# Performance work log

Hardware: AMD Instinct MI355X
Metric: run time of the kernel (lower is better)

## Reference

```python
import jax, jax.numpy as jnp
import numpy as np

NUM_GRAPHS = 256
N_NODES = 100000
N_EDGES = 1200000
NODE_DIM = 64
NUM_LAYERS = 3
R_HID = 128
R_OUT = 32


def setup_inputs() -> dict:
    key = jax.random.key(0)
    ks = jax.random.split(key, 10)
    x = jax.random.normal(ks[0], (N_NODES, NODE_DIM), dtype=jnp.float32)
    src = jax.random.randint(ks[1], (N_EDGES,), 0, N_NODES)
    dst = jax.random.randint(ks[2], (N_EDGES,), 0, N_NODES)
    graph_ids = jnp.sort(jax.random.randint(ks[3], (N_NODES,), 0, NUM_GRAPHS))
    s = 1.0 / np.sqrt(NODE_DIM)
    gin_W = jax.random.normal(ks[4], (NUM_LAYERS, NODE_DIM, NODE_DIM), dtype=jnp.float32) * s
    gin_b = jnp.zeros((NUM_LAYERS, NODE_DIM), dtype=jnp.float32)
    eps = jnp.zeros((NUM_LAYERS,), dtype=jnp.float32)  # learnable GIN epsilon
    in_dim = NODE_DIM * NUM_LAYERS
    r_W1 = jax.random.normal(ks[5], (in_dim, R_HID), dtype=jnp.float32) / np.sqrt(in_dim)
    r_b1 = jnp.zeros((R_HID,), dtype=jnp.float32)
    r_W2 = jax.random.normal(ks[6], (R_HID, R_OUT), dtype=jnp.float32) / np.sqrt(R_HID)
    r_b2 = jnp.zeros((R_OUT,), dtype=jnp.float32)
    return {"x": x, "gin_W": gin_W, "gin_b": gin_b, "eps": eps,
            "r_W1": r_W1, "r_b1": r_b1, "r_W2": r_W2, "r_b2": r_b2,
            "src": src, "dst": dst, "graph_ids": graph_ids}


def reference(x, gin_W, gin_b, eps, r_W1, r_b1, r_W2, r_b2, src, dst, graph_ids):
    n = x.shape[0]
    h = x
    hs = []
    for l in range(NUM_LAYERS):  # fixed small layer loop
        # neighbor sum aggregation: scatter-add messages h[src] into dst
        agg = jax.ops.segment_sum(h[src], dst, num_segments=n)  # [N, D]
        h = jax.nn.relu(((1.0 + eps[l]) * h + agg) @ gin_W[l] + gin_b[l])
        hs.append(h)
    H = jnp.stack(hs, axis=1)  # [N, L, D]
    # dgl.sum_nodes per layer output == ragged segment-sum over graph ids
    g = jax.ops.segment_sum(H, graph_ids, num_segments=NUM_GRAPHS)  # [B, L, D]
    g = g.reshape(NUM_GRAPHS, -1)  # [B, L*D]
    # readout MLP (2 layers)
    out = jax.nn.relu(g @ r_W1 + r_b1) @ r_W2 + r_b2
    return out
```

## Files before the change

### kernel.cpp

```cpp
#include <hip/hip_runtime.h>


#define SPLIT 16
#define NBLK 512
#define BS 512

typedef unsigned short ushort_t;
typedef __bf16 v8bf __attribute__((ext_vector_type(8)));
typedef float v4f __attribute__((ext_vector_type(4)));

__device__ __forceinline__ float h2f_lo(unsigned int v) {
    return (float)__builtin_bit_cast(_Float16, (unsigned short)(v & 0xffffu));
}
__device__ __forceinline__ float h2f_hi(unsigned int v) {
    return (float)__builtin_bit_cast(_Float16, (unsigned short)(v >> 16));
}
__device__ __forceinline__ unsigned int f2h(float f) {
    return (unsigned int)__builtin_bit_cast(unsigned short, (_Float16)f);
}

__global__ void cast_kernel(const float* __restrict__ x, ushort_t* __restrict__ xh, int n4) {
    int i = blockIdx.x * blockDim.x + threadIdx.x;
    if (i < n4) {
        float4 v = ((const float4*)x)[i];
        uint2 p;
        p.x = f2h(v.x) | (f2h(v.y) << 16);
        p.y = f2h(v.z) | (f2h(v.w) << 16);
        ((uint2*)xh)[i] = p;
    }
}

__global__ void prep_w_kernel(const float* __restrict__ W,
                              ushort_t* __restrict__ whi, ushort_t* __restrict__ wlo,
                              int total) {
    int i = blockIdx.x * blockDim.x + threadIdx.x;
    if (i >= total) return;
    int l = i >> 12, r = i & 4095;
    int n = r >> 6, k = r & 63;
    float w = W[l * 4096 + k * 64 + n];
    __bf16 h = (__bf16)w;
    float rem = w - (float)h;
    __bf16 lo = (__bf16)rem;
    whi[i] = __builtin_bit_cast(ushort_t, h);
    wlo[i] = __builtin_bit_cast(ushort_t, lo);
}

__global__ __launch_bounds__(256) void bucket_count_kernel(
        const int* __restrict__ dst, int* __restrict__ cnt2d,
        int E, int nbkt, int ebpb) {
    __shared__ int lcnt[256];
    int t = threadIdx.x;
    lcnt[t] = 0;
    __syncthreads();
    int base = blockIdx.x * ebpb;
    int end = min(base + ebpb, E);
    for (int i = base + t; i < end; i += 256)
        atomicAdd(&lcnt[dst[i] >> 9], 1);
    __syncthreads();
    if (t < nbkt) cnt2d[(size_t)blockIdx.x * nbkt + t] = lcnt[t];
}

__global__ __launch_bounds__(256) void colscan_kernel(
        const int* __restrict__ cnt2d, int* __restrict__ blkoff,
        int* __restrict__ btot, int nbkt) {
    __shared__ int sh[256];
    int b = blockIdx.x, t = threadIdx.x;
    int i0 = 2 * t, i1 = 2 * t + 1;
    int v0 = cnt2d[(size_t)i0 * nbkt + b];
    int v1 = cnt2d[(size_t)i1 * nbkt + b];
    int pair = v0 + v1;
    sh[t] = pair;
    __syncthreads();
    for (int off = 1; off < 256; off <<= 1) {
        int u = (t >= off) ? sh[t - off] : 0;
        __syncthreads();
        sh[t] += u;
        __syncthreads();
    }
    int ex = sh[t] - pair;
    blkoff[(size_t)b * NBLK + i0] = ex;
    blkoff[(size_t)b * NBLK + i1] = ex + v0;
    if (t == 255) btot[b] = sh[255];
}

__global__ __launch_bounds__(256) void bucket_base_kernel(
        const int* __restrict__ btot, int* __restrict__ bbase,
        int* __restrict__ offsets, int nbkt, int N, int E) {
    __shared__ int sh[256];
    int t = threadIdx.x;
    int v = (t < nbkt) ? btot[t] : 0;
    sh[t] = v;
    __syncthreads();
    for (int off = 1; off < 256; off <<= 1) {
        int u = (t >= off) ? sh[t - off] : 0;
        __syncthreads();
        sh[t] += u;
        __syncthreads();
    }
    if (t < nbkt) bbase[t] = sh[t] - v;
    if (t == 0) { bbase[nbkt] = E; offsets[N] = E; }
}

__global__ __launch_bounds__(256) void bucket_scatter_kernel(
        const int* __restrict__ src, const int* __restrict__ dst,
        const int* __restrict__ bbase, const int* __restrict__ blkoff,
        unsigned int* __restrict__ bkt, int E, int nbkt, int ebpb) {
    __shared__ int lbase[256];
    __shared__ int lrank[256];
    int t = threadIdx.x;
    if (t < nbkt) lbase[t] = bbase[t] + blkoff[(size_t)t * NBLK + blockIdx.x];
    lrank[t] = 0;
    __syncthreads();
    int base = blockIdx.x * ebpb;
    int end = min(base + ebpb, E);
    for (int i = base + t; i < end; i += 256) {
        int d = dst[i];
        int b = d >> 9;
        int r = atomicAdd(&lrank[b], 1);
        bkt[lbase[b] + r] = ((unsigned int)src[i] << 9) | (unsigned int)(d & (BS - 1));
    }
}

__global__ __launch_bounds__(256) void csr_build_kernel(
        const unsigned int* __restrict__ bkt, const int* __restrict__ bbase,
        int* __restrict__ offsets, int* __restrict__ csr, int N, int nbkt) {
    __shared__ int cnt[BS];
    __shared__ int rank[BS];
    __shared__ int sh[256];
    int b = blockIdx.x, t = threadIdx.x;
    cnt[t] = 0; cnt[t + 256] = 0;
    rank[t] = 0; rank[t + 256] = 0;
    __syncthreads();
    int base = bbase[b], end = bbase[b + 1];
    for (int i = base + t; i < end; i += 256)
        atomicAdd(&cnt[bkt[i] & (BS - 1)], 1);
    __syncthreads();
    int i0 = 2 * t, i1 = 2 * t + 1;
    int v0 = cnt[i0], v1 = cnt[i1];
    int pair = v0 + v1;
    sh[t] = pair;
    __syncthreads();
    for (int off = 1; off < 256; off <<= 1) {
        int u = (t >= off) ? sh[t - off] : 0;
        __syncthreads();
        sh[t] += u;
        __syncthreads();
    }
    int ex = sh[t] - pair;
    __syncthreads();
    cnt[i0] = ex;
    cnt[i1] = ex + v0;
    __syncthreads();
    int d0 = (b << 9) + i0;
    if (d0 <= N) offsets[d0] = base + cnt[i0];
    int d1 = (b << 9) + i1;
    if (d1 <= N) offsets[d1] = base + cnt[i1];
    for (int i = base + t; i < end; i += 256) {
        unsigned int v = bkt[i];
        int dl = v & (BS - 1);
        int r = atomicAdd(&rank[dl], 1);
        csr[base + cnt[dl] + r] = (int)(v >> 9);
    }
}

__global__ __launch_bounds__(256) void layer_kernel(
        const ushort_t* __restrict__ hin, ushort_t* __restrict__ hout,
        const int* __restrict__ offsets, const int* __restrict__ csr,
        const ushort_t* __restrict__ wt_hi, const ushort_t* __restrict__ wt_lo,
        const float* __restrict__ gin_b, const float* __restrict__ eps_arr,
        int layer, int N) {
    __shared__ float rows[4 * 16 * 64];
    int t = threadIdx.x;
    int wv = t >> 6, lane = t & 63;
    int tile = blockIdx.x * 4 + wv;
    if (tile * 16 >= N) return;
    float* myrows = rows + wv * 16 * 64;
    float eps1 = 1.0f + eps_arr[layer];

    int nq = lane >> 4;
    int sl = lane & 15;

    #pragma unroll
    for (int p = 0; p < 4; ++p) {
        int node = tile * 16 + p * 4 + nq;
        float ax = 0.f, ay = 0.f, az = 0.f, aw = 0.f;
        if (node < N) {
            int e0 = offsets[node], e1 = offsets[node + 1];
            #pragma unroll 4
            for (int e = e0; e < e1; ++e) {
                int s = csr[e];
                uint2 v = ((const uint2*)(hin + (size_t)s * 64))[sl];
                ax += h2f_lo(v.x); ay += h2f_hi(v.x);
                az += h2f_lo(v.y); aw += h2f_hi(v.y);
            }
            uint2 self = ((const uint2*)(hin + (size_t)node * 64))[sl];
            ax = fmaf(eps1, h2f_lo(self.x), ax);
            ay = fmaf(eps1, h2f_hi(self.x), ay);
            az = fmaf(eps1, h2f_lo(self.y), az);
            aw = fmaf(eps1, h2f_hi(self.y), aw);
        }
        float4 r4; r4.x = ax; r4.y = ay; r4.z = az; r4.w = aw;
        *(float4*)&myrows[(p * 4 + nq) * 64 + sl * 4] = r4;
    }

    int c = lane & 15;
    int q = lane >> 4;
    int node16 = tile * 16 + c;

    const ushort_t* Whi = wt_hi + layer * 4096;
    const ushort_t* Wlo = wt_lo + layer * 4096;
    const float*    bl  = gin_b + layer * 64;

    v8bf bhi[2], blo2[2];
    #pragma unroll
    for (int kt = 0; kt < 2; ++kt) {
        float4 f0 = *(float4*)&myrows[c * 64 + kt * 32 + q * 8];
        float4 f1 = *(float4*)&myrows[c * 64 + kt * 32 + q * 8 + 4];
        float xs[8] = {f0.x, f0.y, f0.z, f0.w, f1.x, f1.y, f1.z, f1.w};
        #pragma unroll
        for (int j = 0; j < 8; ++j) {
            __bf16 h = (__bf16)xs[j];
            bhi[kt][j] = h;
            blo2[kt][j] = (__bf16)(xs[j] - (float)h);
        }
    }

    #pragma unroll
    for (int mt = 0; mt < 4; ++mt) {
        v4f acc = {0.f, 0.f, 0.f, 0.f};
        #pragma unroll
        for (int kt = 0; kt < 2; ++kt) {
            int dim = mt * 16 + c;
            size_t off = (size_t)dim * 64 + kt * 32 + q * 8;
            v8bf ah = __builtin_bit_cast(v8bf, *(const uint4*)(Whi + off));
            v8bf al = __builtin_bit_cast(v8bf, *(const uint4*)(Wlo + off));
            acc = __builtin_amdgcn_mfma_f32_16x16x32_bf16(ah, bhi[kt],  acc, 0, 0, 0);
            acc = __builtin_amdgcn_mfma_f32_16x16x32_bf16(ah, blo2[kt], acc, 0, 0, 0);
            acc = __builtin_amdgcn_mfma_f32_16x16x32_bf16(al, bhi[kt],  acc, 0, 0, 0);
        }
        float4 bv = ((const float4*)(bl + mt * 16))[q];
        float o0 = fmaxf(acc[0] + bv.x, 0.f);
        float o1 = fmaxf(acc[1] + bv.y, 0.f);
        float o2 = fmaxf(acc[2] + bv.z, 0.f);
        float o3 = fmaxf(acc[3] + bv.w, 0.f);
        uint2 pk;
        pk.x = f2h(o0) | (f2h(o1) << 16);
        pk.y = f2h(o2) | (f2h(o3) << 16);
        if (node16 < N)
            *(uint2*)(hout + (size_t)node16 * 64 + mt * 16 + q * 4) = pk;
    }
}

__global__ __launch_bounds__(192) void readout_part_kernel(
        const ushort_t* __restrict__ H, const int* __restrict__ gids,
        float* __restrict__ gpart, int N) {
    int graph = blockIdx.x / SPLIT;
    int sp    = blockIdx.x % SPLIT;
    int lo = 0, hi = N;
    while (lo < hi) { int mid = (lo + hi) >> 1; if (gids[mid] < graph) lo = mid + 1; else hi = mid; }
    int start = lo;
    int lo2 = start, hi2 = N;
    while (lo2 < hi2) { int mid = (lo2 + hi2) >> 1; if (gids[mid] < graph + 1) lo2 = mid + 1; else hi2 = mid; }
    int end = lo2;
    int t = threadIdx.x;
    int l = t >> 6, d = t & 63;
    float acc = 0.0f;
    int cnt = end - start;
    if (cnt > 0) {
        int per = (cnt + SPLIT - 1) / SPLIT;
        int cs = start + sp * per;
        int ce = min(cs + per, end);
        const ushort_t* Hl = H + (size_t)l * N * 64;
        for (int n = cs; n < ce; ++n)
            acc += (float)__builtin_bit_cast(_Float16, Hl[(size_t)n * 64 + d]);
    }
    gpart[(size_t)(graph * SPLIT + sp) * 192 + t] = acc;
}

__global__ __launch_bounds__(192) void mlp_kernel(
        const float* __restrict__ gpart,
        const float* __restrict__ W1, const float* __restrict__ b1,
        const float* __restrict__ W2, const float* __restrict__ b2,
        float* __restrict__ out) {
    __shared__ float gr[192];
    __shared__ float hid[128];
    int graph = blockIdx.x;
    int t = threadIdx.x;
    float a = 0.f;
    #pragma unroll
    for (int sp = 0; sp < SPLIT; ++sp)
        a += gpart[(size_t)(graph * SPLIT + sp) * 192 + t];
    gr[t] = a;
    __syncthreads();
    if (t < 128) {
        float s = b1[t];
        for (int k = 0; k < 192; ++k) s = fmaf(gr[k], W1[k * 128 + t], s);
        hid[t] = fmaxf(s, 0.0f);
    }
    __syncthreads();
    if (t < 32) {
        float s = b2[t];
        for (int k = 0; k < 128; ++k) s = fmaf(hid[k], W2[k * 32 + t], s);
        out[graph * 32 + t] = s;
    }
}

extern "C" void kernel_launch(void* const* d_in, const int* in_sizes, int n_in,
                              void* d_out, int out_size, void* d_ws, size_t ws_size,
                              hipStream_t stream) {
    const float* x     = (const float*)d_in[0];
    const float* gin_W = (const float*)d_in[1];
    const float* gin_b = (const float*)d_in[2];
    const float* eps   = (const float*)d_in[3];
    const float* r_W1  = (const float*)d_in[4];
    const float* r_b1  = (const float*)d_in[5];
    const float* r_W2  = (const float*)d_in[6];
    const float* r_b2  = (const float*)d_in[7];
    const int*   src   = (const int*)d_in[8];
    const int*   dst   = (const int*)d_in[9];
    const int*   gids  = (const int*)d_in[10];

    int N = in_sizes[0] / 64;
    int E = in_sizes[8];
    int B = out_size / 32;

    int nbkt = (N + BS - 1) / BS;
    int ebpb = (E + NBLK - 1) / NBLK;

    int* ws       = (int*)d_ws;
    float* gpart  = (float*)ws;
    int* cnt2d    = ws + (size_t)B * SPLIT * 192;
    int* blkoff   = cnt2d + (size_t)NBLK * nbkt;
    int* btot     = blkoff + (size_t)nbkt * NBLK;
    int* bbase    = btot + nbkt;
    int* offsets  = bbase + (nbkt + 1);
    unsigned int* bkt = (unsigned int*)(offsets + (N + 1));
    int* csr      = (int*)(bkt + E);
    size_t w      = (size_t)(csr + E - ws);
    w = (w + 15) & ~(size_t)15;
    ushort_t* xh  = (ushort_t*)(ws + w);
    ushort_t* H   = xh + (size_t)N * 64;
    ushort_t* whi = H + 3 * (size_t)N * 64;
    ushort_t* wlo = whi + 3 * 4096;

    cast_kernel<<<(N * 64 / 4 + 255) / 256, 256, 0, stream>>>(x, xh, N * 64 / 4);
    prep_w_kernel<<<(3 * 4096 + 255) / 256, 256, 0, stream>>>(gin_W, whi, wlo, 3 * 4096);
    bucket_count_kernel<<<NBLK, 256, 0, stream>>>(dst, cnt2d, E, nbkt, ebpb);
    colscan_kernel<<<nbkt, 256, 0, stream>>>(cnt2d, blkoff, btot, nbkt);
    bucket_base_kernel<<<1, 256, 0, stream>>>(btot, bbase, offsets, nbkt, N, E);
    bucket_scatter_kernel<<<NBLK, 256, 0, stream>>>(src, dst, bbase, blkoff, bkt, E, nbkt, ebpb);
    csr_build_kernel<<<nbkt, 256, 0, stream>>>(bkt, bbase, offsets, csr, N, nbkt);

    int lbk = (N + 63) / 64;
    ushort_t* H0 = H;
    ushort_t* H1 = H + (size_t)N * 64;
    ushort_t* H2 = H + 2 * (size_t)N * 64;

    layer_kernel<<<lbk, 256, 0, stream>>>(xh, H0, offsets, csr, whi, wlo, gin_b, eps, 0, N);
    layer_kernel<<<lbk, 256, 0, stream>>>(H0, H1, offsets, csr, whi, wlo, gin_b, eps, 1, N);
    layer_kernel<<<lbk, 256, 0, stream>>>(H1, H2, offsets, csr, whi, wlo, gin_b, eps, 2, N);

    readout_part_kernel<<<B * SPLIT, 192, 0, stream>>>(H, gids, gpart, N);
    mlp_kernel<<<B, 192, 0, stream>>>(gpart, r_W1, r_b1, r_W2, r_b2, (float*)d_out);
}
```

Baseline: 326.1 us.

## Fuse prep kernels and restructure GIN layer to one tile per block

Merges the cast, weight-prep and bucket-count kernels into a single launch by dispatching on block index, which saves two launches. The layer kernel now gives each block one 16-node tile. Each wave gathers 4 nodes in a single pass instead of looping over 16 serially, then computes one 16-wide output slice of the matmul after a block barrier. Neighbour indices are preloaded cooperatively into registers and broadcast with shuffles. This is meant to raise memory-level parallelism and shorten per-wave latency chains, at the cost of a block barrier and four times as many blocks.

```diff
diff --git a/kernel.cpp b/kernel.cpp
--- a/kernel.cpp
+++ b/kernel.cpp
@@ -19,45 +19,45 @@
     return (unsigned int)__builtin_bit_cast(unsigned short, (_Float16)f);
 }
 
-__global__ void cast_kernel(const float* __restrict__ x, ushort_t* __restrict__ xh, int n4) {
-    int i = blockIdx.x * blockDim.x + threadIdx.x;
-    if (i < n4) {
-        float4 v = ((const float4*)x)[i];
-        uint2 p;
-        p.x = f2h(v.x) | (f2h(v.y) << 16);
-        p.y = f2h(v.z) | (f2h(v.w) << 16);
-        ((uint2*)xh)[i] = p;
-    }
-}
-
-__global__ void prep_w_kernel(const float* __restrict__ W,
-                              ushort_t* __restrict__ whi, ushort_t* __restrict__ wlo,
-                              int total) {
-    int i = blockIdx.x * blockDim.x + threadIdx.x;
-    if (i >= total) return;
-    int l = i >> 12, r = i & 4095;
-    int n = r >> 6, k = r & 63;
-    float w = W[l * 4096 + k * 64 + n];
-    __bf16 h = (__bf16)w;
-    float rem = w - (float)h;
-    __bf16 lo = (__bf16)rem;
-    whi[i] = __builtin_bit_cast(ushort_t, h);
-    wlo[i] = __builtin_bit_cast(ushort_t, lo);
-}
-
-__global__ __launch_bounds__(256) void bucket_count_kernel(
+__global__ __launch_bounds__(256) void pre_kernel(
         const int* __restrict__ dst, int* __restrict__ cnt2d,
-        int E, int nbkt, int ebpb) {
+        int E, int nbkt, int ebpb,
+        const float* __restrict__ x, ushort_t* __restrict__ xh, int n4, int castBlocks,
+        const float* __restrict__ W, ushort_t* __restrict__ whi,
+        ushort_t* __restrict__ wlo, int wtotal) {
     __shared__ int lcnt[256];
     int t = threadIdx.x;
-    lcnt[t] = 0;
-    __syncthreads();
-    int base = blockIdx.x * ebpb;
-    int end = min(base + ebpb, E);
-    for (int i = base + t; i < end; i += 256)
-        atomicAdd(&lcnt[dst[i] >> 9], 1);
-    __syncthreads();
-    if (t < nbkt) cnt2d[(size_t)blockIdx.x * nbkt + t] = lcnt[t];
+    int blk = blockIdx.x;
+    if (blk < NBLK) {
+        lcnt[t] = 0;
+        __syncthreads();
+        int base = blk * ebpb;
+        int end = min(base + ebpb, E);
+        for (int i = base + t; i < end; i += 256)
+            atomicAdd(&lcnt[dst[i] >> 9], 1);
+        __syncthreads();
+        if (t < nbkt) cnt2d[(size_t)blk * nbkt + t] = lcnt[t];
+    } else if (blk < NBLK + castBlocks) {
+        int i = (blk - NBLK) * 256 + t;
+        if (i < n4) {
+            float4 v = ((const float4*)x)[i];
+            uint2 p;
+            p.x = f2h(v.x) | (f2h(v.y) << 16);
+            p.y = f2h(v.z) | (f2h(v.w) << 16);
+            ((uint2*)xh)[i] = p;
+        }
+    } else {
+        int i = (blk - NBLK - castBlocks) * 256 + t;
+        if (i < wtotal) {
+            int l = i >> 12, r = i & 4095;
+            int n = r >> 6, k = r & 63;
+            float w = W[l * 4096 + k * 64 + n];
+            __bf16 h = (__bf16)w;
+            float rem = w - (float)h;
+            whi[i] = __builtin_bit_cast(ushort_t, h);
+            wlo[i] = __builtin_bit_cast(ushort_t, (__bf16)rem);
+        }
+    }
 }
 
 __global__ __launch_bounds__(256) void colscan_kernel(
@@ -169,43 +169,59 @@
         const ushort_t* __restrict__ wt_hi, const ushort_t* __restrict__ wt_lo,
         const float* __restrict__ gin_b, const float* __restrict__ eps_arr,
         int layer, int N) {
-    __shared__ float rows[4 * 16 * 64];
+    __shared__ float rows[16 * 64];
     int t = threadIdx.x;
     int wv = t >> 6, lane = t & 63;
-    int tile = blockIdx.x * 4 + wv;
-    if (tile * 16 >= N) return;
-    float* myrows = rows + wv * 16 * 64;
+    int tile = blockIdx.x;
     float eps1 = 1.0f + eps_arr[layer];
 
     int nq = lane >> 4;
     int sl = lane & 15;
-
-    #pragma unroll
-    for (int p = 0; p < 4; ++p) {
-        int node = tile * 16 + p * 4 + nq;
-        float ax = 0.f, ay = 0.f, az = 0.f, aw = 0.f;
-        if (node < N) {
-            int e0 = offsets[node], e1 = offsets[node + 1];
-            #pragma unroll 4
-            for (int e = e0; e < e1; ++e) {
-                int s = csr[e];
-                uint2 v = ((const uint2*)(hin + (size_t)s * 64))[sl];
-                ax += h2f_lo(v.x); ay += h2f_hi(v.x);
-                az += h2f_lo(v.y); aw += h2f_hi(v.y);
-            }
-            uint2 self = ((const uint2*)(hin + (size_t)node * 64))[sl];
-            ax = fmaf(eps1, h2f_lo(self.x), ax);
-            ay = fmaf(eps1, h2f_hi(self.x), ay);
-            az = fmaf(eps1, h2f_lo(self.y), az);
-            aw = fmaf(eps1, h2f_hi(self.y), aw);
-        }
-        float4 r4; r4.x = ax; r4.y = ay; r4.z = az; r4.w = aw;
-        *(float4*)&myrows[(p * 4 + nq) * 64 + sl * 4] = r4;
-    }
+    int gbase = lane & 48;
+
+    int node = tile * 16 + wv * 4 + nq;
+    float ax = 0.f, ay = 0.f, az = 0.f, aw = 0.f;
+    if (node < N) {
+        int a = offsets[node], b = offsets[node + 1];
+        int deg = b - a;
+        int idxA = (sl < deg) ? csr[a + sl] : 0;
+        int idxB = (16 + sl < deg) ? csr[a + 16 + sl] : 0;
+        int d1 = min(deg, 16);
+        #pragma unroll 8
+        for (int j = 0; j < d1; ++j) {
+            int s = __shfl(idxA, gbase + j, 64);
+            uint2 v = ((const uint2*)(hin + (size_t)s * 64))[sl];
+            ax += h2f_lo(v.x); ay += h2f_hi(v.x);
+            az += h2f_lo(v.y); aw += h2f_hi(v.y);
+        }
+        int d2 = min(deg, 32);
+        #pragma unroll 8
+        for (int j = 16; j < d2; ++j) {
+            int s = __shfl(idxB, gbase + (j - 16), 64);
+            uint2 v = ((const uint2*)(hin + (size_t)s * 64))[sl];
+            ax += h2f_lo(v.x); ay += h2f_hi(v.x);
+            az += h2f_lo(v.y); aw += h2f_hi(v.y);
+        }
+        for (int e = a + 32; e < b; ++e) {
+            int s = csr[e];
+            uint2 v = ((const uint2*)(hin + (size_t)s * 64))[sl];
+            ax += h2f_lo(v.x); ay += h2f_hi(v.x);
+            az += h2f_lo(v.y); aw += h2f_hi(v.y);
+        }
+        uint2 self = ((const uint2*)(hin + (size_t)node * 64))[sl];
+        ax = fmaf(eps1, h2f_lo(self.x), ax);
+        ay = fmaf(eps1, h2f_hi(self.x), ay);
+        az = fmaf(eps1, h2f_lo(self.y), az);
+        aw = fmaf(eps1, h2f_hi(self.y), aw);
+    }
+    float4 r4; r4.x = ax; r4.y = ay; r4.z = az; r4.w = aw;
+    *(float4*)&rows[(wv * 4 + nq) * 64 + sl * 4] = r4;
+    __syncthreads();
 
     int c = lane & 15;
     int q = lane >> 4;
     int node16 = tile * 16 + c;
+    int mt = wv;
 
     const ushort_t* Whi = wt_hi + layer * 4096;
     const ushort_t* Wlo = wt_lo + layer * 4096;
@@ -214,8 +230,8 @@
     v8bf bhi[2], blo2[2];
     #pragma unroll
     for (int kt = 0; kt < 2; ++kt) {
-        float4 f0 = *(float4*)&myrows[c * 64 + kt * 32 + q * 8];
-        float4 f1 = *(float4*)&myrows[c * 64 + kt * 32 + q * 8 + 4];
+        float4 f0 = *(float4*)&rows[c * 64 + kt * 32 + q * 8];
+        float4 f1 = *(float4*)&rows[c * 64 + kt * 32 + q * 8 + 4];
         float xs[8] = {f0.x, f0.y, f0.z, f0.w, f1.x, f1.y, f1.z, f1.w};
         #pragma unroll
         for (int j = 0; j < 8; ++j) {
@@ -225,30 +241,27 @@
         }
     }
 
+    v4f acc = {0.f, 0.f, 0.f, 0.f};
     #pragma unroll
-    for (int mt = 0; mt < 4; ++mt) {
-        v4f acc = {0.f, 0.f, 0.f, 0.f};
-        #pragma unroll
-        for (int kt = 0; kt < 2; ++kt) {
-            int dim = mt * 16 + c;
-            size_t off = (size_t)dim * 64 + kt * 32 + q * 8;
-            v8bf ah = __builtin_bit_cast(v8bf, *(const uint4*)(Whi + off));
-            v8bf al = __builtin_bit_cast(v8bf, *(const uint4*)(Wlo + off));
-            acc = __builtin_amdgcn_mfma_f32_16x16x32_bf16(ah, bhi[kt],  acc, 0, 0, 0);
-            acc = __builtin_amdgcn_mfma_f32_16x16x32_bf16(ah, blo2[kt], acc, 0, 0, 0);
-            acc = __builtin_amdgcn_mfma_f32_16x16x32_bf16(al, bhi[kt],  acc, 0, 0, 0);
-        }
-        float4 bv = ((const float4*)(bl + mt * 16))[q];
-        float o0 = fmaxf(acc[0] + bv.x, 0.f);
-        float o1 = fmaxf(acc[1] + bv.y, 0.f);
-        float o2 = fmaxf(acc[2] + bv.z, 0.f);
-        float o3 = fmaxf(acc[3] + bv.w, 0.f);
-        uint2 pk;
-        pk.x = f2h(o0) | (f2h(o1) << 16);
-        pk.y = f2h(o2) | (f2h(o3) << 16);
-        if (node16 < N)
-            *(uint2*)(hout + (size_t)node16 * 64 + mt * 16 + q * 4) = pk;
-    }
+    for (int kt = 0; kt < 2; ++kt) {
+        int dim = mt * 16 + c;
+        size_t off = (size_t)dim * 64 + kt * 32 + q * 8;
+        v8bf ah = __builtin_bit_cast(v8bf, *(const uint4*)(Whi + off));
+        v8bf al = __builtin_bit_cast(v8bf, *(const uint4*)(Wlo + off));
+        acc = __builtin_amdgcn_mfma_f32_16x16x32_bf16(ah, bhi[kt],  acc, 0, 0, 0);
+        acc = __builtin_amdgcn_mfma_f32_16x16x32_bf16(ah, blo2[kt], acc, 0, 0, 0);
+        acc = __builtin_amdgcn_mfma_f32_16x16x32_bf16(al, bhi[kt],  acc, 0, 0, 0);
+    }
+    float4 bv = ((const float4*)(bl + mt * 16))[q];
+    float o0 = fmaxf(acc[0] + bv.x, 0.f);
+    float o1 = fmaxf(acc[1] + bv.y, 0.f);
+    float o2 = fmaxf(acc[2] + bv.z, 0.f);
+    float o3 = fmaxf(acc[3] + bv.w, 0.f);
+    uint2 pk;
+    pk.x = f2h(o0) | (f2h(o1) << 16);
+    pk.y = f2h(o2) | (f2h(o3) << 16);
+    if (node16 < N)
+        *(uint2*)(hout + (size_t)node16 * 64 + mt * 16 + q * 4) = pk;
 }
 
 __global__ __launch_bounds__(192) void readout_part_kernel(
@@ -326,6 +339,10 @@
 
     int nbkt = (N + BS - 1) / BS;
     int ebpb = (E + NBLK - 1) / NBLK;
+    int n4 = N * 64 / 4;
+    int castBlocks = (n4 + 255) / 256;
+    int wtotal = 3 * 4096;
+    int prepBlocks = (wtotal + 255) / 256;
 
     int* ws       = (int*)d_ws;
     float* gpart  = (float*)ws;
@@ -343,15 +360,14 @@
     ushort_t* whi = H + 3 * (size_t)N * 64;
     ushort_t* wlo = whi + 3 * 4096;
 
-    cast_kernel<<<(N * 64 / 4 + 255) / 256, 256, 0, stream>>>(x, xh, N * 64 / 4);
-    prep_w_kernel<<<(3 * 4096 + 255) / 256, 256, 0, stream>>>(gin_W, whi, wlo, 3 * 4096);
-    bucket_count_kernel<<<NBLK, 256, 0, stream>>>(dst, cnt2d, E, nbkt, ebpb);
+    pre_kernel<<<NBLK + castBlocks + prepBlocks, 256, 0, stream>>>(
+        dst, cnt2d, E, nbkt, ebpb, x, xh, n4, castBlocks, gin_W, whi, wlo, wtotal);
     colscan_kernel<<<nbkt, 256, 0, stream>>>(cnt2d, blkoff, btot, nbkt);
     bucket_base_kernel<<<1, 256, 0, stream>>>(btot, bbase, offsets, nbkt, N, E);
     bucket_scatter_kernel<<<NBLK, 256, 0, stream>>>(src, dst, bbase, blkoff, bkt, E, nbkt, ebpb);
     csr_build_kernel<<<nbkt, 256, 0, stream>>>(bkt, bbase, offsets, csr, N, nbkt);
 
-    int lbk = (N + 63) / 64;
+    int lbk = (N + 15) / 16;
     ushort_t* H0 = H;
     ushort_t* H1 = H + (size_t)N * 64;
     ushort_t* H2 = H + 2 * (size_t)N * 64;
```

New measurement: 334.0 us. +2.4%, slower.
